# Performance work log

Measured on AMD Instinct MI355X. Metric: run time of the kernel, lower is better.

## Reference

```python
import jax, jax.numpy as jnp
import numpy as np

D_MODEL = 1024
D_INNER = 2048
D_STATE = 16
D_CONV = 4
DT_RANK = 64  # ceil(D_MODEL / 16)
BATCH = 2
SEQLEN = 2048


def setup_inputs() -> dict:
    key = jax.random.key(0)
    ks = jax.random.split(key, 9)
    s = 0.02
    hidden_states = jax.random.normal(ks[0], (BATCH, SEQLEN, D_MODEL), dtype=jnp.float32)
    W_in = jax.random.normal(ks[1], (D_MODEL, 2 * D_INNER), dtype=jnp.float32) * s
    # flax depthwise Conv kernel layout: (window, in_features//groups=1, out_features)
    conv_kernel = jax.random.normal(ks[2], (D_CONV, 1, D_INNER), dtype=jnp.float32) * 0.2
    conv_bias = jax.random.normal(ks[3], (D_INNER,), dtype=jnp.float32) * s
    W_x = jax.random.normal(ks[4], (D_INNER, DT_RANK + 2 * D_STATE), dtype=jnp.float32) * s
    W_dt = jax.random.normal(ks[5], (DT_RANK, D_INNER), dtype=jnp.float32) * s
    b_dt = jax.random.normal(ks[6], (D_INNER,), dtype=jnp.float32) * s
    # A_log = log(arange(1, d_state+1)) broadcast over d_inner (constant init in module)
    A_log = jnp.log(jnp.broadcast_to(jnp.arange(1, D_STATE + 1, dtype=jnp.float32), (D_INNER, D_STATE)))
    D = jnp.ones((D_INNER,), dtype=jnp.float32)
    W_out = jax.random.normal(ks[7], (D_INNER, D_MODEL), dtype=jnp.float32) * s
    return {
        "hidden_states": hidden_states,
        "W_in": W_in,
        "conv_kernel": conv_kernel,
        "conv_bias": conv_bias,
        "W_x": W_x,
        "W_dt": W_dt,
        "b_dt": b_dt,
        "A_log": A_log,
        "D": D,
        "W_out": W_out,
    }


def _mamba_forward(hidden_states, W_in, conv_kernel, conv_bias, W_x, W_dt, b_dt, A_log, D, W_out):
    # in_proj, then einops '(d i)' split with i=2 => interleaved channels
    xz = hidden_states @ W_in                       # (b, l, 2*d_inner)
    x = xz[..., 0::2]                               # (b, l, d_inner)
    z = xz[..., 1::2]                               # (b, l, d_inner)

    # depthwise conv1d, padding='SAME' (as in flax nn.Conv)
    x = jax.lax.conv_general_dilated(
        x, conv_kernel, window_strides=(1,), padding="SAME",
        dimension_numbers=("NWC", "WIO", "NWC"),
        feature_group_count=D_INNER,
    ) + conv_bias
    x = jax.nn.silu(x)

    x_dbl = x @ W_x                                 # (b, l, dt_rank + 2*d_state)
    dt = x_dbl[..., :DT_RANK] @ W_dt + b_dt         # (b, l, d_inner)
    Bm = x_dbl[..., DT_RANK:DT_RANK + D_STATE]      # (b, l, n)
    Cm = x_dbl[..., DT_RANK + D_STATE:]             # (b, l, n)

    A = -jnp.exp(A_log.astype(jnp.float32))         # (d_inner, n)
    delta = jax.nn.softplus(dt.astype(jnp.float32)) # (b, l, d_inner)

    deltaA = jnp.exp(jnp.einsum("bld,dn->lbdn", delta, A))          # (l, b, d, n)
    deltaB_u = jnp.einsum("bld,bln,bld->lbdn", delta, Bm, x)        # (l, b, d, n)
    C_l = jnp.transpose(Cm, (1, 0, 2))                               # (l, b, n)

    state0 = jnp.zeros((BATCH, D_INNER, D_STATE), dtype=jnp.float32)

    def step(state, inputs):
        dA, dBu, c = inputs
        state = dA * state + dBu                    # (b, d, n)
        y = jnp.einsum("bdn,bn->bd", state, c)      # (b, d)
        return state, y

    _, y = jax.lax.scan(step, state0, (deltaA, deltaB_u, C_l))
    y = jnp.transpose(y, (1, 0, 2))                 # (b, l, d_inner)

    out = (y + x * D) * jax.nn.silu(z)              # skip via D, gate via silu(z)
    return out @ W_out                              # (b, l, d_model)


def reference(hidden_states, W_in, conv_kernel, conv_bias, W_x, W_dt, b_dt, A_log, D, W_out):
    return _mamba_forward(hidden_states, W_in, conv_kernel, conv_bias, W_x, W_dt, b_dt, A_log, D, W_out)
```

## Files before the change

### kernel.cpp

```cpp
#include <hip/hip_runtime.h>
#include <hip/hip_bf16.h>

typedef unsigned short u16;
typedef __attribute__((ext_vector_type(8))) short short8;
typedef __attribute__((ext_vector_type(4))) short short4v;
typedef __attribute__((ext_vector_type(4))) float f32x4;
typedef __attribute__((ext_vector_type(4))) float float4v;
typedef __attribute__((ext_vector_type(2))) float f32x2;

#define DMODEL 1024
#define DI 2048
#define NST 16
#define RANK 64
#define BB 2
#define LL 2048
#define MM (BB*LL)
#define LC 32
#define NCH (LL/LC)

__device__ __forceinline__ float b2f(u16 v){ union{unsigned u; float f;}x; x.u=(unsigned)v<<16; return x.f; }
__device__ __forceinline__ u16 f2b(float f){
  union{unsigned u; float f;}x; x.f=f;
  unsigned r = x.u + 0x7FFFu + ((x.u>>16)&1u);
  return (u16)(r>>16);
}
__device__ __forceinline__ bool probe_bf(const u16* probe){ return probe[1] != 0; }
__device__ __forceinline__ float ldin(const void* p, size_t i, bool bf){
  return bf ? b2f(((const u16*)p)[i]) : ((const float*)p)[i];
}
__device__ __forceinline__ u16 ldb(const void* p, size_t i, bool bf){
  return bf ? ((const u16*)p)[i] : f2b(((const float*)p)[i]);
}
__device__ __forceinline__ void gl16(const u16* g, char* lds_wave_base){
  __builtin_amdgcn_global_load_lds((const __attribute__((address_space(1))) unsigned*)g,
                                   (__attribute__((address_space(3))) unsigned*)lds_wave_base, 16, 0, 0);
}

template<int EPI>
__global__ __launch_bounds__(512,2) void mgemm256_k(
    const u16* __restrict__ A, const u16* __restrict__ Bt,
    void* __restrict__ O0, void* __restrict__ O1,
    int M, int N, int K, int lda, int ldb, int ldc)
{
  __shared__ char smem[131072];
  const int t = threadIdx.x;
  int bx = blockIdx.x, by = blockIdx.y;
  {
    const int gx = gridDim.x;
    const int nwg = gx*gridDim.y;
    const int lin = by*gx + bx;
    const int swz = (lin & 7)*(nwg>>3) + (lin>>3);
    bx = swz % gx; by = swz / gx;
  }
  const int m0 = by*256, n0 = bx*256;
  const int kbeg = blockIdx.z * K;
  const int wv = t >> 6, ln = t & 63;
  const int wr = wv >> 2, wc = wv & 3;
  const int lr = ln & 15, q = ln >> 4;
  const int NT = K >> 6;

  const int srow8 = ln >> 3;
  const int koff = ((ln & 7) ^ srow8) * 8;
  auto stA = [&](int kt, int h){
    char* d = smem + (kt&1)*65536 + h*16384;
    const u16* g = A + (size_t)(m0 + h*128 + wv*8 + srow8)*lda + kbeg + kt*64 + koff;
    gl16(g, d + wv*1024);
    gl16(g + (size_t)64*lda, d + 8192 + wv*1024);
  };
  auto stB = [&](int kt, int h){
    char* d = smem + (kt&1)*65536 + 32768 + h*16384;
    const u16* g = Bt + (size_t)(n0 + h*128 + wv*8 + srow8)*ldb + kbeg + kt*64 + koff;
    gl16(g, d + wv*1024);
    gl16(g + (size_t)64*ldb, d + 8192 + wv*1024);
  };

  int arow[8], brow[4], ck[2];
#pragma unroll
  for(int s=0;s<8;s++)  arow[s] = (s>>2)*16384 + (wr*16 + (s&3)*32 + lr)*128;
#pragma unroll
  for(int s2=0;s2<4;s2++) brow[s2] = 32768 + (s2>>1)*16384 + (wc*16 + (s2&1)*64 + lr)*128;
#pragma unroll
  for(int ks=0;ks<2;ks++) ck[ks] = ((ks*4 + q) ^ (lr & 7)) * 16;

  f32x4 acc[8][4];
#pragma unroll
  for(int i=0;i<8;i++)
#pragma unroll
    for(int j=0;j<4;j++) acc[i][j] = (f32x4){0.f,0.f,0.f,0.f};

  stA(0,0); stB(0,0); stA(0,1); stB(0,1);
  stA(1,0); stB(1,0);
  asm volatile("s_waitcnt vmcnt(4)" ::: "memory");
  __builtin_amdgcn_sched_barrier(0);
  __builtin_amdgcn_s_barrier();
  __builtin_amdgcn_sched_barrier(0);

  short8 aR[4][2], b0R[2][2], b1R[2][2];
  for(int kt=0; kt<NT; ++kt){
    const char* base = smem + (kt&1)*65536;
#pragma unroll
    for(int s=0;s<4;s++)
#pragma unroll
      for(int ks=0;ks<2;ks++) aR[s][ks] = *(const short8*)(base + arow[s] + ck[ks]);
#pragma unroll
    for(int j=0;j<2;j++)
#pragma unroll
      for(int ks=0;ks<2;ks++) b0R[j][ks] = *(const short8*)(base + brow[j] + ck[ks]);
    if(kt+1 < NT) stA(kt+1, 1);
    __builtin_amdgcn_s_barrier();
    asm volatile("s_waitcnt lgkmcnt(0)" ::: "memory");
    __builtin_amdgcn_sched_barrier(0);
    __builtin_amdgcn_s_setprio(1);
#pragma unroll
    for(int s=0;s<4;s++)
#pragma unroll
      for(int j=0;j<2;j++)
#pragma unroll
        for(int ks=0;ks<2;ks++)
          acc[s][j] = __builtin_amdgcn_mfma_f32_16x16x32_bf16(aR[s][ks], b0R[j][ks], acc[s][j], 0,0,0);
    __builtin_amdgcn_s_setprio(0);
    __builtin_amdgcn_s_barrier();
    __builtin_amdgcn_sched_barrier(0);
#pragma unroll
    for(int j=0;j<2;j++)
#pragma unroll
      for(int ks=0;ks<2;ks++) b1R[j][ks] = *(const short8*)(base + brow[2+j] + ck[ks]);
    if(kt+1 < NT) stB(kt+1, 1);
    __builtin_amdgcn_s_barrier();
    asm volatile("s_waitcnt lgkmcnt(0)" ::: "memory");
    __builtin_amdgcn_sched_barrier(0);
    __builtin_amdgcn_s_setprio(1);
#pragma unroll
    for(int s=0;s<4;s++)
#pragma unroll
      for(int j=0;j<2;j++)
#pragma unroll
        for(int ks=0;ks<2;ks++)
          acc[s][2+j] = __builtin_amdgcn_mfma_f32_16x16x32_bf16(aR[s][ks], b1R[j][ks], acc[s][2+j], 0,0,0);
    __builtin_amdgcn_s_setprio(0);
    __builtin_amdgcn_s_barrier();
    __builtin_amdgcn_sched_barrier(0);
#pragma unroll
    for(int s=0;s<4;s++)
#pragma unroll
      for(int ks=0;ks<2;ks++) aR[s][ks] = *(const short8*)(base + arow[4+s] + ck[ks]);
    if(kt+2 < NT) stA(kt+2, 0);
    __builtin_amdgcn_s_barrier();
    asm volatile("s_waitcnt lgkmcnt(0)" ::: "memory");
    __builtin_amdgcn_sched_barrier(0);
    __builtin_amdgcn_s_setprio(1);
#pragma unroll
    for(int s=0;s<4;s++)
#pragma unroll
      for(int j=0;j<2;j++)
#pragma unroll
        for(int ks=0;ks<2;ks++)
          acc[4+s][j] = __builtin_amdgcn_mfma_f32_16x16x32_bf16(aR[s][ks], b0R[j][ks], acc[4+s][j], 0,0,0);
    __builtin_amdgcn_s_setprio(0);
    __builtin_amdgcn_s_barrier();
    __builtin_amdgcn_sched_barrier(0);
    if(kt+2 < NT){
      stB(kt+2, 0);
      asm volatile("s_waitcnt vmcnt(4)" ::: "memory");
    } else if(kt+1 < NT){
      asm volatile("s_waitcnt vmcnt(0)" ::: "memory");
    }
    __builtin_amdgcn_sched_barrier(0);
    __builtin_amdgcn_s_barrier();
    __builtin_amdgcn_sched_barrier(0);
    __builtin_amdgcn_s_setprio(1);
#pragma unroll
    for(int s=0;s<4;s++)
#pragma unroll
      for(int j=0;j<2;j++)
#pragma unroll
        for(int ks=0;ks<2;ks++)
          acc[4+s][2+j] = __builtin_amdgcn_mfma_f32_16x16x32_bf16(aR[s][ks], b1R[j][ks], acc[4+s][2+j], 0,0,0);
    __builtin_amdgcn_s_setprio(0);
    __builtin_amdgcn_s_barrier();
    __builtin_amdgcn_sched_barrier(0);
  }

  if(EPI==4){
    u16* tile = (u16*)smem;
    u16* obase = (n0 < DI) ? (u16*)O0 : (u16*)O1;
    const int cb = n0 & (DI-1);
    for(int h=0;h<2;h++){
      __builtin_amdgcn_s_barrier();
#pragma unroll
      for(int s=0;s<4;s++)
#pragma unroll
        for(int r=0;r<4;r++){
          int trow = wr*16 + s*32 + q*4 + r;
#pragma unroll
          for(int s2=0;s2<4;s2++)
            tile[trow*264 + wc*16 + s2*64 + lr] = f2b(acc[h*4+s][s2][r]);
        }
      asm volatile("s_waitcnt lgkmcnt(0)" ::: "memory");
      __builtin_amdgcn_sched_barrier(0);
      __builtin_amdgcn_s_barrier();
      __builtin_amdgcn_sched_barrier(0);
#pragma unroll
      for(int it=0;it<8;it++){
        int idx = it*512 + t;
        int row = idx >> 5;
        int ch  = (idx & 31) * 8;
        short8 v = *(const short8*)(tile + row*264 + ch);
        *(short8*)(obase + (size_t)(m0 + h*128 + row)*ldc + cb + ch) = v;
      }
    }
    return;
  }
#pragma unroll
  for(int s=0;s<8;s++){
#pragma unroll
    for(int r=0;r<4;r++){
      int row = m0 + wr*16 + s*32 + q*4 + r;
#pragma unroll
      for(int s2=0;s2<4;s2++){
        int col = n0 + wc*16 + s2*64 + lr;
        ((float*)O0)[(size_t)blockIdx.z*M*ldc + (size_t)row*ldc + col] = acc[s][s2][r];
      }
    }
  }
}

template<int EPI>
__global__ __launch_bounds__(256,2) void mgemm_k(
    const u16* __restrict__ A, const u16* __restrict__ Bt,
    void* __restrict__ O0, void* __restrict__ O1,
    const void* __restrict__ bias, const u16* __restrict__ probe,
    int M, int N, int K, int lda, int ldb, int ldc)
{
  __shared__ char smem[16384];
  const int t = threadIdx.x;
  int bx = blockIdx.x, by = blockIdx.y;
  {
    const int gx = gridDim.x;
    const int nwg = gx*gridDim.y;
    const int lin = by*gx + bx;
    const int swz = (lin & 7)*(nwg>>3) + (lin>>3);
    bx = swz % gx; by = swz / gx;
  }
  const int m0 = by*128, n0 = bx*128;
  const int kbeg = blockIdx.z * K;
  const int lane = t & 63;
  const int wv = t >> 6;
  const int wm = (wv>>1)*64, wn = (wv&1)*64;
  const int lr = lane & 15, q = lane >> 4;

  const int r0 = t>>2, q0 = t&3;
  const u16* Ag0 = A + kbeg + (size_t)(m0 + r0)*lda + q0*8;
  const u16* Ag1 = A + kbeg + (size_t)(m0 + 64 + r0)*lda + q0*8;
  const u16* Bg0 = Bt + kbeg + (size_t)(n0 + r0)*ldb + q0*8;
  const u16* Bg1 = Bt + kbeg + (size_t)(n0 + 64 + r0)*ldb + q0*8;
  char* const wbase = smem + (t & ~63)*16;
  char* const lA0 = wbase;
  char* const lA1 = wbase + 4096;
  char* const lB0 = wbase + 8192;
  char* const lB1 = wbase + 12288;

  int aro[4], bro[4];
#pragma unroll
  for(int i=0;i<4;i++) aro[i] = (wm + i*16 + lr)*64 + q*16;
#pragma unroll
  for(int j=0;j<4;j++) bro[j] = (wn + j*16 + lr)*64 + q*16;

  f32x4 acc[4][4];
#pragma unroll
  for(int i=0;i<4;i++)
#pragma unroll
    for(int j=0;j<4;j++) acc[i][j] = (f32x4){0.f,0.f,0.f,0.f};

  for(int k0=0;k0<K;k0+=32){
    __syncthreads();
    gl16(Ag0 + k0, lA0); gl16(Ag1 + k0, lA1);
    gl16(Bg0 + k0, lB0); gl16(Bg1 + k0, lB1);
    __syncthreads();
    short8 af[4], bfv[4];
#pragma unroll
    for(int i=0;i<4;i++) af[i] = *(const short8*)(smem + aro[i]);
#pragma unroll
    for(int j=0;j<4;j++) bfv[j] = *(const short8*)(smem + 8192 + bro[j]);
#pragma unroll
    for(int i=0;i<4;i++)
#pragma unroll
      for(int j=0;j<4;j++)
        acc[i][j] = __builtin_amdgcn_mfma_f32_16x16x32_bf16(af[i], bfv[j], acc[i][j], 0,0,0);
  }

#pragma unroll
  for(int i=0;i<4;i++){
#pragma unroll
    for(int r=0;r<4;r++){
      int row = m0 + wm + i*16 + q*4 + r;
#pragma unroll
      for(int j=0;j<4;j++){
        int col = n0 + wn + j*16 + lr;
        ((float*)O0)[(size_t)blockIdx.z*M*ldc + (size_t)row*ldc + col] = acc[i][j][r];
      }
    }
  }
}

__global__ __launch_bounds__(256,2) void dt_k(
    const u16* __restrict__ A,
    const u16* __restrict__ Bt,
    u16* __restrict__ O,
    const void* __restrict__ bias, const u16* __restrict__ probe)
{
  const bool bf = probe_bf(probe);
  __shared__ char smem[33792];
  const int t = threadIdx.x;
  int bx = blockIdx.x, by = blockIdx.y;
  {
    const int gx = gridDim.x;
    const int nwg = gx*gridDim.y;
    const int lin = by*gx + bx;
    const int swz = (lin & 7)*(nwg>>3) + (lin>>3);
    bx = swz % gx; by = swz / gx;
  }
  const int m0 = by*128, n0 = bx*128;
  const int lane = t & 63, wv = t >> 6;
  const int wm = (wv>>1)*64, wn = (wv&1)*64;
  const int lr = lane & 15, q = lane >> 4;

  const int srow = t >> 3;
  const int koff = (((t&7) ^ (srow&7)) * 8);
  const u16* gA = A  + (size_t)(m0 + srow)*128 + koff;
  const u16* gB = Bt + (size_t)(n0 + srow)*64  + koff;
  char* const lA = smem + wv*1024;
  char* const lB = smem + 16384 + wv*1024;
#pragma unroll
  for(int r=0;r<4;r++){
    gl16(gA + (size_t)r*32*128, lA + r*4096);
    gl16(gB + (size_t)r*32*64,  lB + r*4096);
  }
  __syncthreads();

  f32x4 acc[4][4];
#pragma unroll
  for(int i=0;i<4;i++)
#pragma unroll
    for(int j=0;j<4;j++) acc[i][j] = (f32x4){0.f,0.f,0.f,0.f};

#pragma unroll
  for(int ks=0;ks<2;ks++){
    short8 af[4], bfv[4];
#pragma unroll
    for(int i=0;i<4;i++){
      int row = wm + i*16 + lr;
      af[i] = *(const short8*)(smem + row*128 + (((ks*4+q) ^ (row&7))*16));
    }
#pragma unroll
    for(int j=0;j<4;j++){
      int row = wn + j*16 + lr;
      bfv[j] = *(const short8*)(smem + 16384 + row*128 + (((ks*4+q) ^ (row&7))*16));
    }
#pragma unroll
    for(int i=0;i<4;i++)
#pragma unroll
      for(int j=0;j<4;j++)
        acc[i][j] = __builtin_amdgcn_mfma_f32_16x16x32_bf16(af[i], bfv[j], acc[i][j], 0,0,0);
  }

  float bj[4];
#pragma unroll
  for(int j=0;j<4;j++) bj[j] = ldin(bias, n0 + wn + j*16 + lr, bf);
  __syncthreads();
  u16* tile = (u16*)smem;
#pragma unroll
  for(int i=0;i<4;i++)
#pragma unroll
    for(int r=0;r<4;r++){
      int trow = wm + i*16 + q*4 + r;
#pragma unroll
      for(int j=0;j<4;j++){
        int tcol = wn + j*16 + lr;
        float s = acc[i][j][r] + bj[j];
        float e = __expf(-fabsf(s));
        float sp = fmaxf(s, 0.f) + __logf(1.f + e);
        tile[trow*132 + tcol] = f2b(sp);
      }
    }
  __syncthreads();
#pragma unroll
  for(int it=0;it<8;it++){
    int idx = it*256 + t;
    int row = idx >> 4;
    int colc = (idx & 15) * 8;
    short8 v = *(const short8*)(tile + row*132 + colc);
    *(short8*)(O + (size_t)(m0+row)*DI + n0 + colc) = v;
  }
}

__device__ __forceinline__ void tr_block(
    const void* src, u16* dst, int R, int C, int bx, int by, bool bf, bool perm,
    int tid, u16 (*tile)[33])
{
  const int c0 = bx*32, r0 = by*32;
  const int tc = tid & 31, tr0 = tid >> 5;
#pragma unroll
  for(int i=0;i<4;i++){
    int r = tr0 + i*8;
    int gc = c0 + tc;
    tile[r][tc] = (gc < C) ? ldb(src, (size_t)(r0+r)*C + gc, bf) : (u16)0;
  }
  __syncthreads();
#pragma unroll
  for(int i=0;i<4;i++){
    int dr = c0 + tr0 + i*8;
    if(perm) dr = (dr>>1) + ((dr&1)<<11);
    int dc = r0 + tc;
    dst[(size_t)dr*R + dc] = tile[tc][tr0 + i*8];
  }
}

__global__ __launch_bounds__(256) void prep_k(
    const void* __restrict__ W_in, const void* __restrict__ W_out,
    const void* __restrict__ W_x, const void* __restrict__ W_dt,
    const void* __restrict__ hidden,
    u16* __restrict__ WinT, u16* __restrict__ WoutT, u16* __restrict__ WxT,
    u16* __restrict__ WdtT, u16* __restrict__ hb, const u16* __restrict__ probe)
{
  const bool bf = probe_bf(probe);
  __shared__ u16 tile[32][33];
  const int bid = blockIdx.x, t = threadIdx.x;
  if(bid < 4096){
    tr_block(W_in, WinT, DMODEL, 2*DI, bid & 127, bid >> 7, bf, true, t, tile);
  } else if(bid < 6144){
    int b2 = bid - 4096; tr_block(W_out, WoutT, DI, DMODEL, b2 & 31, b2 >> 5, bf, false, t, tile);
  } else if(bid < 6400){
    int b2 = bid - 6144; tr_block(W_x, WxT, DI, 96, b2 & 3, b2 >> 2, bf, false, t, tile);
  } else if(bid < 6528){
    int b2 = bid - 6400; tr_block(W_dt, WdtT, RANK, DI, b2 & 63, b2 >> 6, bf, false, t, tile);
  } else {
    size_t i = ((size_t)(bid - 6528)*256 + t)*8;
    if(bf){
      *(short8*)(hb+i) = *(const short8*)((const u16*)hidden + i);
    } else {
      float4v a = *(const float4v*)((const float*)hidden + i);
      float4v b = *(const float4v*)((const float*)hidden + i + 4);
      short8 r;
      r[0]=(short)f2b(a[0]); r[1]=(short)f2b(a[1]); r[2]=(short)f2b(a[2]); r[3]=(short)f2b(a[3]);
      r[4]=(short)f2b(b[0]); r[5]=(short)f2b(b[1]); r[6]=(short)f2b(b[2]); r[7]=(short)f2b(b[3]);
      *(short8*)(hb+i) = r;
    }
  }
}

__global__ __launch_bounds__(256) void redx_k(
    const float* __restrict__ P, float* __restrict__ xdbl, u16* __restrict__ xdblb)
{
  size_t i = ((size_t)blockIdx.x*256 + threadIdx.x)*4;
  float4v s = *(const float4v*)(P + i);
#pragma unroll
  for(int p=1;p<8;p++) s += *(const float4v*)(P + (size_t)p*MM*128 + i);
  *(float4v*)(xdbl + i) = s;
  short4v r; r[0]=(short)f2b(s[0]); r[1]=(short)f2b(s[1]); r[2]=(short)f2b(s[2]); r[3]=(short)f2b(s[3]);
  *(short4v*)(xdblb + i) = r;
}

__global__ __launch_bounds__(256) void red7_k(
    const float* __restrict__ P, void* __restrict__ out, const u16* __restrict__ probe)
{
  const bool bf = probe_bf(probe);
  size_t i = ((size_t)blockIdx.x*256 + threadIdx.x)*4;
  float4v s = *(const float4v*)(P + i);
#pragma unroll
  for(int p=1;p<4;p++) s += *(const float4v*)(P + (size_t)p*MM*DMODEL + i);
  if(bf){
    short4v r; r[0]=(short)f2b(s[0]); r[1]=(short)f2b(s[1]); r[2]=(short)f2b(s[2]); r[3]=(short)f2b(s[3]);
    *(short4v*)((u16*)out + i) = r;
  } else {
    *(float4v*)((float*)out + i) = s;
  }
}

__global__ __launch_bounds__(256) void conv_silu_k(
  const u16* __restrict__ xb, const void* __restrict__ w,
  const void* __restrict__ bias, u16* __restrict__ xcb,
  const u16* __restrict__ probe)
{
  const bool bf = probe_bf(probe);
  const int row = blockIdx.x;
  const int tt = row & (LL-1);
  const int d = threadIdx.x*8;
  float wv[4][8], bv[8];
  if(bf){
    short8 bb = *(const short8*)((const u16*)bias + d);
#pragma unroll
    for(int j=0;j<8;j++) bv[j] = b2f((u16)bb[j]);
#pragma unroll
    for(int k=0;k<4;k++){
      short8 ww = *(const short8*)((const u16*)w + k*DI + d);
#pragma unroll
      for(int j=0;j<8;j++) wv[k][j] = b2f((u16)ww[j]);
    }
  } else {
    *(float4v*)(bv)   = *(const float4v*)((const float*)bias + d);
    *(float4v*)(bv+4) = *(const float4v*)((const float*)bias + d + 4);
#pragma unroll
    for(int k=0;k<4;k++){
      *(float4v*)(wv[k])   = *(const float4v*)((const float*)w + k*DI + d);
      *(float4v*)(wv[k]+4) = *(const float4v*)((const float*)w + k*DI + d + 4);
    }
  }
  float acc[8];
#pragma unroll
  for(int j=0;j<8;j++) acc[j] = bv[j];
  const u16* xrow = xb + (size_t)row*DI + d;
#pragma unroll
  for(int k=0;k<4;k++){
    int o = tt - 1 + k;
    if(0<=o && o<LL){
      short8 xv = *(const short8*)(xrow + (ptrdiff_t)(k-1)*DI);
#pragma unroll
      for(int j=0;j<8;j++) acc[j] = fmaf(b2f((u16)xv[j]), wv[k][j], acc[j]);
    }
  }
  short8 sb;
#pragma unroll
  for(int j=0;j<8;j++){ float s = acc[j] / (1.f + __expf(-acc[j])); sb[j]=(short)f2b(s); }
  *(short8*)(xcb + (size_t)row*DI + d) = sb;
}

__global__ __launch_bounds__(256,4) void scan_a_k(
  const u16* __restrict__ dlb, const u16* __restrict__ xcb,
  const float* __restrict__ xdbl, const void* __restrict__ A_log,
  float* __restrict__ Bacc, float* __restrict__ sumdv,
  const u16* __restrict__ probe)
{
  const bool bf = probe_bf(probe);
  __shared__ float Bsh[LC][NST];
  const int t = threadIdx.x;
  const int d0 = blockIdx.x*256 + t;
  const int b = blockIdx.y, c = blockIdx.z;
  for(int i=t;i<LC*NST;i+=256){
    int l = i>>4, n = i&15;
    Bsh[l][n] = xdbl[((size_t)b*LL + (size_t)c*LC + l)*128 + 64 + n];
  }
  __syncthreads();
  float ac[NST], s[NST];
#pragma unroll
  for(int n=0;n<NST;n++){
    ac[n] = -__expf(ldin(A_log, (size_t)d0*NST+n, bf));
    s[n]=0.f;
  }
  bool geom = true;
  {
    float a0 = ac[0];
#pragma unroll
    for(int n=1;n<NST;n++) geom = geom && (fabsf(ac[n]-(n+1)*a0) <= 1e-4f*(n+1)*fabsf(a0));
  }
  float sum=0.f;
  const size_t base0 = ((size_t)b*LL + (size_t)c*LC)*DI + d0;
  const u16* dptr = dlb + base0;
  const u16* xptr = xcb + base0;

  auto stepA = [&](int l, u16 dp, u16 xp){
    float dv=b2f(dp), xv=b2f(xp);
    float du=dv*xv;
    sum+=dv;
    if(geom){
      float e=__expf(ac[0]*dv);
      float p=1.f;
#pragma unroll
      for(int n=0;n<NST;n++){
        p*=e; s[n]=fmaf(p, s[n], du*Bsh[l][n]);
      }
    } else {
#pragma unroll
      for(int n=0;n<NST;n++)
        s[n]=fmaf(__expf(ac[n]*dv), s[n], du*Bsh[l][n]);
    }
  };

  u16 dpA = dptr[0], xpA = xptr[0];
  u16 dpB = dptr[DI], xpB = xptr[DI];
  for(int l=0;l<LC;l+=2){
    int l2 = (l+2 < LC) ? l+2 : LC-1;
    int l3 = (l+3 < LC) ? l+3 : LC-1;
    u16 dpC = dptr[(size_t)l2*DI], xpC = xptr[(size_t)l2*DI];
    u16 dpD = dptr[(size_t)l3*DI], xpD = xptr[(size_t)l3*DI];
    stepA(l,   dpA, xpA);
    stepA(l+1, dpB, xpB);
    dpA=dpC; xpA=xpC; dpB=dpD; xpB=xpD;
  }

  const size_t ob = ((size_t)c*BB + b)*((size_t)NST*DI) + d0;
#pragma unroll
  for(int n=0;n<NST;n++) Bacc[ob + (size_t)n*DI] = s[n];
  sumdv[((size_t)c*BB + b)*DI + d0] = sum;
}

__global__ __launch_bounds__(256) void scan_b_k(
  const float* __restrict__ Bacc, const float* __restrict__ sumdv,
  const void* __restrict__ A_log, float* __restrict__ Sin,
  const u16* __restrict__ probe)
{
  const bool bf = probe_bf(probe);
  const int idx = blockIdx.x*256 + threadIdx.x;
  const int d = idx & (DI-1);
  const int n = (idx >> 11) & 15;
  const int b = idx >> 15;
  const float ac = -__expf(ldin(A_log, (size_t)d*NST+n, bf));
  float s = 0.f;
  float svN = sumdv[((size_t)0*BB + b)*DI + d];
  float bbN = Bacc[idx];
  for(int c=0;c<NCH;c++){
    int c1 = (c+1 < NCH) ? c+1 : NCH-1;
    float svC = sumdv[((size_t)c1*BB + b)*DI + d];
    float bbC = Bacc[(size_t)c1*((size_t)BB*NST*DI) + idx];
    float a = __expf(ac * svN);
    Sin[(size_t)c*((size_t)BB*NST*DI) + idx] = s;
    s = fmaf(a, s, bbN);
    svN = svC; bbN = bbC;
  }
}

__global__ __launch_bounds__(256,4) void scan_c_gate_k(
  const u16* __restrict__ dlb, const u16* __restrict__ xcb,
  const float* __restrict__ xdbl, const void* __restrict__ A_log,
  const float* __restrict__ Sin, const u16* __restrict__ zb,
  const void* __restrict__ Dw, u16* __restrict__ G,
  const u16* __restrict__ probe)
{
  const bool bf = probe_bf(probe);
  __shared__ float Bsh[LC][NST], Csh[LC][NST];
  const int t = threadIdx.x;
  const int d0 = blockIdx.x*256 + t;
  const int b = blockIdx.y, c = blockIdx.z;
  for(int i=t;i<LC*NST;i+=256){
    int l = i>>4, n = i&15;
    size_t ro = ((size_t)b*LL + (size_t)c*LC + l)*128;
    Bsh[l][n] = xdbl[ro + 64 + n];
    Csh[l][n] = xdbl[ro + 80 + n];
  }
  __syncthreads();
  float ac[NST], s[NST];
  const size_t ib = ((size_t)c*BB + b)*((size_t)NST*DI) + d0;
#pragma unroll
  for(int n=0;n<NST;n++)
    ac[n] = -__expf(ldin(A_log, (size_t)d0*NST+n, bf));
#pragma unroll
  for(int n=0;n<NST;n++) s[n] = Sin[ib + (size_t)n*DI];
  bool geom = true;
  {
    float a0 = ac[0];
#pragma unroll
    for(int n=1;n<NST;n++) geom = geom && (fabsf(ac[n]-(n+1)*a0) <= 1e-4f*(n+1)*fabsf(a0));
  }
  const float D0 = ldin(Dw, d0, bf);
  const size_t base0 = ((size_t)b*LL + (size_t)c*LC)*DI + d0;
  const u16* dptr = dlb + base0;
  const u16* xptr = xcb + base0;
  const u16* zptr = zb  + base0;

  auto stepC = [&](int l, u16 dp, u16 xp, u16 zz){
    float dv=b2f(dp), xv=b2f(xp);
    float du=dv*xv;
    float y=0.f;
    if(geom){
      float e=__expf(ac[0]*dv);
      float p=1.f;
#pragma unroll
      for(int n=0;n<NST;n++){
        p*=e; s[n]=fmaf(p, s[n], du*Bsh[l][n]); y=fmaf(s[n], Csh[l][n], y);
      }
    } else {
#pragma unroll
      for(int n=0;n<NST;n++){
        s[n]=fmaf(__expf(ac[n]*dv), s[n], du*Bsh[l][n]); y=fmaf(s[n], Csh[l][n], y);
      }
    }
    float z0 = b2f(zz);
    float g0 = z0 / (1.f + __expf(-z0));
    float o0 = (y + xv*D0) * g0;
    G[base0 + (size_t)l*DI] = f2b(o0);
  };

  u16 dpA = dptr[0], xpA = xptr[0], zzA = zptr[0];
  u16 dpB = dptr[DI], xpB = xptr[DI], zzB = zptr[DI];
  for(int l=0;l<LC;l+=2){
    int l2 = (l+2 < LC) ? l+2 : LC-1;
    int l3 = (l+3 < LC) ? l+3 : LC-1;
    u16 dpC = dptr[(size_t)l2*DI], xpC = xptr[(size_t)l2*DI], zzC = zptr[(size_t)l2*DI];
    u16 dpD = dptr[(size_t)l3*DI], xpD = xptr[(size_t)l3*DI], zzD = zptr[(size_t)l3*DI];
    stepC(l,   dpA, xpA, zzA);
    stepC(l+1, dpB, xpB, zzB);
    dpA=dpC; xpA=xpC; zzA=zzC; dpB=dpD; xpB=xpD; zzB=zzD;
  }
}

extern "C" void kernel_launch(void* const* d_in, const int* in_sizes, int n_in,
                              void* d_out, int out_size, void* d_ws, size_t ws_size,
                              hipStream_t stream)
{
  const void* hidden = d_in[0];
  const void* W_in   = d_in[1];
  const void* convw  = d_in[2];
  const void* convb  = d_in[3];
  const void* W_x    = d_in[4];
  const void* W_dt   = d_in[5];
  const void* b_dt   = d_in[6];
  const u16*  A_log  = (const u16*)d_in[7];
  const void* Dw     = d_in[8];
  const void* W_out  = d_in[9];

  char* p = (char*)d_ws;
  u16*   xb   = (u16*)  p;
  float* Sin  = (float*)p;
  float* Pw7  = (float*)p;
  u16*   zb   = (u16*)  (p + 16777216);
  u16*   xcb  = (u16*)  (p + 33554432);
  float* Bcc  = (float*)(p + 67108864);
  u16*   G    = (u16*)  (p + 83886080);
  float* Pw   = (float*)(p + 100663296);
  u16*   dlb  = (u16*)  (p + 100663296);
  u16*   hb   = (u16*)  (p + 117440512);
  float* sumdv= (float*)(p + 117440512);
  float* xdbl = (float*)(p + 134217728);
  u16*   xdblb= (u16*)  (p + 136314880);
  u16*   WinT = (u16*)  (p + 137363456);
  u16*   WoutT= (u16*)  (p + 145752064);
  u16*   WxT  = (u16*)  (p + 149946368);
  u16*   WdtT = (u16*)  (p + 150470656);

  prep_k<<<6528 + (MM*DMODEL)/(256*8), 256, 0, stream>>>(
      W_in, W_out, W_x, W_dt, hidden, WinT, WoutT, WxT, WdtT, hb, A_log);
  mgemm256_k<4><<<dim3(16,16), 512, 0, stream>>>(hb, WinT, xb, zb,
                                                 MM, 2*DI, DMODEL, DMODEL, DMODEL, DI);
  conv_silu_k<<<MM, 256, 0, stream>>>(xb, convw, convb, xcb, A_log);
  mgemm_k<1><<<dim3(1,32,8), 256, 0, stream>>>(xcb, WxT, Pw, nullptr, nullptr, A_log,
                                               MM, 128, DI/8, DI, DI, 128);
  redx_k<<<(MM*128)/(256*4), 256, 0, stream>>>(Pw, xdbl, xdblb);
  dt_k<<<dim3(16,32), 256, 0, stream>>>(xdblb, WdtT, dlb, b_dt, A_log);
  scan_a_k<<<dim3(DI/256, BB, NCH), 256, 0, stream>>>(dlb, xcb, xdbl, A_log, Bcc, sumdv, A_log);
  scan_b_k<<<(BB*NST*DI)/256, 256, 0, stream>>>(Bcc, sumdv, A_log, Sin, A_log);
  scan_c_gate_k<<<dim3(DI/256, BB, NCH), 256, 0, stream>>>(dlb, xcb, xdbl, A_log, Sin, zb, Dw, G, A_log);
  mgemm256_k<1><<<dim3(4,16,4), 512, 0, stream>>>(G, WoutT, Pw7, nullptr,
                                                  MM, DMODEL, DI/4, DI, DI, DMODEL);
  red7_k<<<(MM*DMODEL)/(256*4), 256, 0, stream>>>(Pw7, d_out, A_log);
}
```

Before: 285.5 us.

## Replace split-K out-projection GEMM and reduction with single full-K GEMM

```diff
diff --git a/kernel.cpp b/kernel.cpp
--- a/kernel.cpp
+++ b/kernel.cpp
@@ -289,6 +289,24 @@
         acc[i][j] = __builtin_amdgcn_mfma_f32_16x16x32_bf16(af[i], bfv[j], acc[i][j], 0,0,0);
   }
 
+  if(EPI==2){
+    const bool bf = probe_bf(probe);
+#pragma unroll
+    for(int i=0;i<4;i++){
+#pragma unroll
+      for(int r=0;r<4;r++){
+        int row = m0 + wm + i*16 + q*4 + r;
+#pragma unroll
+        for(int j=0;j<4;j++){
+          int col = n0 + wn + j*16 + lr;
+          float v = acc[i][j][r];
+          if(bf) ((u16*)O0)[(size_t)row*ldc + col] = f2b(v);
+          else   ((float*)O0)[(size_t)row*ldc + col] = v;
+        }
+      }
+    }
+    return;
+  }
 #pragma unroll
   for(int i=0;i<4;i++){
 #pragma unroll
@@ -461,22 +479,6 @@
   *(short4v*)(xdblb + i) = r;
 }
 
-__global__ __launch_bounds__(256) void red7_k(
-    const float* __restrict__ P, void* __restrict__ out, const u16* __restrict__ probe)
-{
-  const bool bf = probe_bf(probe);
-  size_t i = ((size_t)blockIdx.x*256 + threadIdx.x)*4;
-  float4v s = *(const float4v*)(P + i);
-#pragma unroll
-  for(int p=1;p<4;p++) s += *(const float4v*)(P + (size_t)p*MM*DMODEL + i);
-  if(bf){
-    short4v r; r[0]=(short)f2b(s[0]); r[1]=(short)f2b(s[1]); r[2]=(short)f2b(s[2]); r[3]=(short)f2b(s[3]);
-    *(short4v*)((u16*)out + i) = r;
-  } else {
-    *(float4v*)((float*)out + i) = s;
-  }
-}
-
 __global__ __launch_bounds__(256) void conv_silu_k(
   const u16* __restrict__ xb, const void* __restrict__ w,
   const void* __restrict__ bias, u16* __restrict__ xcb,
@@ -711,7 +713,6 @@
   char* p = (char*)d_ws;
   u16*   xb   = (u16*)  p;
   float* Sin  = (float*)p;
-  float* Pw7  = (float*)p;
   u16*   zb   = (u16*)  (p + 16777216);
   u16*   xcb  = (u16*)  (p + 33554432);
   float* Bcc  = (float*)(p + 67108864);
@@ -739,7 +740,6 @@
   scan_a_k<<<dim3(DI/256, BB, NCH), 256, 0, stream>>>(dlb, xcb, xdbl, A_log, Bcc, sumdv, A_log);
   scan_b_k<<<(BB*NST*DI)/256, 256, 0, stream>>>(Bcc, sumdv, A_log, Sin, A_log);
   scan_c_gate_k<<<dim3(DI/256, BB, NCH), 256, 0, stream>>>(dlb, xcb, xdbl, A_log, Sin, zb, Dw, G, A_log);
-  mgemm256_k<1><<<dim3(4,16,4), 512, 0, stream>>>(G, WoutT, Pw7, nullptr,
-                                                  MM, DMODEL, DI/4, DI, DI, DMODEL);
-  red7_k<<<(MM*DMODEL)/(256*4), 256, 0, stream>>>(Pw7, d_out, A_log);
-}
+  mgemm_k<2><<<dim3(DMODEL/128, MM/128), 256, 0, stream>>>(G, WoutT, d_out, nullptr, nullptr, A_log,
+                                                           MM, DMODEL, DI, DI, DI, DMODEL);
+}
```

Result: slower. 292.0 us (+2.3%).
